# Performance work log

Hardware: AMD Instinct MI355X
Metric: run time of the kernel (lower is better)

Reference implementation:

```python
import jax, jax.numpy as jnp
import numpy as np

N_HEADS = 16
N_EMBD = 1024
HEAD_SIZE = N_EMBD // N_HEADS
B, T = 4, 2048
EPS = 1e-5


def _layernorm(x, g, b):
    mu = jnp.mean(x, axis=-1, keepdims=True)
    var = jnp.mean((x - mu) ** 2, axis=-1, keepdims=True)
    return (x - mu) * jax.lax.rsqrt(var + EPS) * g + b


def setup_inputs() -> dict:
    key = jax.random.key(0)
    ks = jax.random.split(key, 12)
    s_in = 1.0 / np.sqrt(N_EMBD)
    s_ff = 1.0 / np.sqrt(4 * N_EMBD)
    return {
        "x": jax.random.normal(ks[0], (B, T, N_EMBD), jnp.float32),
        "Wq": jax.random.normal(ks[1], (N_HEADS, N_EMBD, HEAD_SIZE), jnp.float32) * s_in,
        "Wk": jax.random.normal(ks[2], (N_HEADS, N_EMBD, HEAD_SIZE), jnp.float32) * s_in,
        "Wv": jax.random.normal(ks[3], (N_HEADS, N_EMBD, HEAD_SIZE), jnp.float32) * s_in,
        "Wproj": jax.random.normal(ks[4], (N_EMBD, N_EMBD), jnp.float32) * s_in,
        "bproj": jnp.zeros((N_EMBD,), jnp.float32),
        "ln1_g": jnp.ones((N_EMBD,), jnp.float32),
        "ln1_b": jnp.zeros((N_EMBD,), jnp.float32),
        "ln2_g": jnp.ones((N_EMBD,), jnp.float32),
        "ln2_b": jnp.zeros((N_EMBD,), jnp.float32),
        "W1": jax.random.normal(ks[5], (N_EMBD, 4 * N_EMBD), jnp.float32) * s_in,
        "b1": jnp.zeros((4 * N_EMBD,), jnp.float32),
        "W2": jax.random.normal(ks[6], (4 * N_EMBD, N_EMBD), jnp.float32) * s_ff,
        "b2": jnp.zeros((N_EMBD,), jnp.float32),
    }


def reference(x, Wq, Wk, Wv, Wproj, bproj, ln1_g, ln1_b, ln2_g, ln2_b, W1, b1, W2, b2):
    Bx, Tx, C = x.shape
    # --- self-attention on ln1(x) ---
    h = _layernorm(x, ln1_g, ln1_b)
    q = jnp.einsum('btc,hcd->bhtd', h, Wq)
    k = jnp.einsum('btc,hcd->bhtd', h, Wk)
    v = jnp.einsum('btc,hcd->bhtd', h, Wv)
    # NOTE: original scales by C**-0.5 where C = n_embd (full dim), not head_size
    scores = jnp.einsum('bhtd,bhsd->bhts', q, k) * (C ** -0.5)
    causal = jnp.tril(jnp.ones((Tx, Tx), dtype=bool))
    scores = jnp.where(causal, scores, -jnp.inf)
    wei = jax.nn.softmax(scores, axis=-1)
    attn = jnp.einsum('bhts,bhsd->bhtd', wei, v)  # [B,H,T,hs]
    attn = attn.transpose(0, 2, 1, 3).reshape(Bx, Tx, -1)  # concat heads -> [B,T,C]
    x = x + attn @ Wproj + bproj
    # --- feed-forward on ln2(x) ---
    h2 = _layernorm(x, ln2_g, ln2_b)
    ff = jax.nn.relu(h2 @ W1 + b1) @ W2 + b2
    return x + ff
```

## Files before the change

kernel.cpp:

```cpp
#include <hip/hip_runtime.h>
#include <math.h>

typedef short bf16x8 __attribute__((ext_vector_type(8)));
typedef float f32x4 __attribute__((ext_vector_type(4)));
typedef unsigned short u16;

__device__ __forceinline__ u16 f2bf(float f) {
    union { float f; unsigned u; } v; v.f = f;
    unsigned r = v.u + 0x7fffu + ((v.u >> 16) & 1u);
    return (u16)(r >> 16);
}

__device__ __forceinline__ void gload_lds16(const void* g, void* l) {
    __builtin_amdgcn_global_load_lds((const __attribute__((address_space(1))) void*)g,
                                     (__attribute__((address_space(3))) void*)l, 16, 0, 0);
}

__global__ __launch_bounds__(256)
void transpose_cvt(const float* __restrict__ in, u16* __restrict__ out, int R, int C)
{
    __shared__ float tile[64][65];
    const size_t slab = (size_t)blockIdx.z * R * C;
    const float* ip = in + slab;
    u16* op = out + slab;
    const int r0 = blockIdx.y * 64, c0 = blockIdx.x * 64;
    const int t = threadIdx.x;
    const int tr = t >> 6, tc = t & 63;
    #pragma unroll
    for (int i = 0; i < 16; ++i)
        tile[tr + i*4][tc] = ip[(size_t)(r0 + tr + i*4)*C + c0 + tc];
    __syncthreads();
    #pragma unroll
    for (int i = 0; i < 16; ++i)
        op[(size_t)(c0 + tr + i*4)*R + r0 + tc] = f2bf(tile[tc][tr + i*4]);
}

__global__ __launch_bounds__(256)
void ln_kernel(const float* __restrict__ x, const float* __restrict__ g,
               const float* __restrict__ b, u16* __restrict__ out)
{
    const int row = blockIdx.x;
    const int t = threadIdx.x;
    const float4 v = ((const float4*)(x + (size_t)row*1024))[t];
    float s = v.x + v.y + v.z + v.w;
    float ss = v.x*v.x + v.y*v.y + v.z*v.z + v.w*v.w;
    #pragma unroll
    for (int m = 1; m < 64; m <<= 1) {
        s  += __shfl_xor(s, m);
        ss += __shfl_xor(ss, m);
    }
    __shared__ float red[8];
    const int wave = t >> 6;
    if ((t & 63) == 0) { red[wave] = s; red[4 + wave] = ss; }
    __syncthreads();
    s  = red[0] + red[1] + red[2] + red[3];
    ss = red[4] + red[5] + red[6] + red[7];
    const float mu = s * (1.f/1024.f);
    const float rs = rsqrtf(ss * (1.f/1024.f) - mu*mu + 1e-5f);
    const float4 gv = ((const float4*)g)[t];
    const float4 bv = ((const float4*)b)[t];
    ushort4 ov;
    ov.x = f2bf((v.x - mu)*rs*gv.x + bv.x);
    ov.y = f2bf((v.y - mu)*rs*gv.y + bv.y);
    ov.z = f2bf((v.z - mu)*rs*gv.z + bv.z);
    ov.w = f2bf((v.w - mu)*rs*gv.w + bv.w);
    ((ushort4*)(out + (size_t)row*1024))[t] = ov;
}

template<int NWG, int N, int K, int EPI>
__global__ __launch_bounds__(256)
void gemm_kernel(const u16* __restrict__ A, const u16* __restrict__ BT,
                 float* __restrict__ out_f32, u16* __restrict__ out_bf16,
                 const float* __restrict__ bias, const float* __restrict__ res,
                 u16* __restrict__ qbuf, u16* __restrict__ kbuf, u16* __restrict__ vt)
{
    __shared__ u16 As[128*32];
    __shared__ u16 Bs[128*32];
    const int bid = blockIdx.x;
    const int tid = ((bid & 7) * (NWG / 8)) + (bid >> 3);
    const int m0 = (tid & 63) * 128;
    const int n0 = (tid >> 6) * 128;
    const int t = threadIdx.x;
    const int wave = t >> 6;
    const int lane = t & 63;
    const int l15 = lane & 15, lg = lane >> 4;
    const int wr = wave >> 1, wc = wave & 1;
    f32x4 acc[4][4] = {};

    const int srow = t >> 2;
    const int sce  = (t & 3) * 8;
    for (int k0 = 0; k0 < K; k0 += 32) {
        #pragma unroll
        for (int i = 0; i < 2; ++i) {
            const u16* ga = A  + (size_t)(m0 + i*64 + srow) * K + k0 + sce;
            const u16* gb = BT + (size_t)(n0 + i*64 + srow) * K + k0 + sce;
            gload_lds16(ga, As + i*2048 + wave*512);
            gload_lds16(gb, Bs + i*2048 + wave*512);
        }
        __syncthreads();
        bf16x8 af[4], bfr[4];
        #pragma unroll
        for (int mi = 0; mi < 4; ++mi)
            af[mi] = *(const bf16x8*)(As + (wr*64 + mi*16 + l15)*32 + lg*8);
        #pragma unroll
        for (int ni = 0; ni < 4; ++ni)
            bfr[ni] = *(const bf16x8*)(Bs + (wc*64 + ni*16 + l15)*32 + lg*8);
        #pragma unroll
        for (int mi = 0; mi < 4; ++mi)
            #pragma unroll
            for (int ni = 0; ni < 4; ++ni)
                acc[mi][ni] = __builtin_amdgcn_mfma_f32_16x16x32_bf16(af[mi], bfr[ni], acc[mi][ni], 0, 0, 0);
        __syncthreads();
    }

    #pragma unroll
    for (int mi = 0; mi < 4; ++mi) {
        #pragma unroll
        for (int ni = 0; ni < 4; ++ni) {
            const int gc = n0 + wc*64 + ni*16 + l15;
            #pragma unroll
            for (int j = 0; j < 4; ++j) {
                const int gr = m0 + wr*64 + mi*16 + lg*4 + j;
                float v = acc[mi][ni][j];
                if constexpr (EPI == 0) {
                    u16 bv = f2bf(v);
                    if (gc < 1024) {
                        qbuf[(size_t)gr*1024 + gc] = bv;
                    } else if (gc < 2048) {
                        kbuf[(size_t)gr*1024 + (gc - 1024)] = bv;
                    } else {
                        const int hd = gc - 2048;
                        const int bb = gr >> 11, tt = gr & 2047;
                        vt[(size_t)((bb*16 + (hd >> 6))*64 + (hd & 63))*2048 + tt] = bv;
                    }
                } else if constexpr (EPI == 1) {
                    out_f32[(size_t)gr*N + gc] = v + bias[gc] + res[(size_t)gr*N + gc];
                } else {
                    out_bf16[(size_t)gr*N + gc] = f2bf(fmaxf(v + bias[gc], 0.f));
                }
            }
        }
    }
}

__device__ __forceinline__ void attn_qtile(
    bf16x8 (&qf)[2][2], f32x4 (&o)[2][4], float (&mprev)[2][4], float (&lsum)[2][4],
    const u16* Ksc, const u16* Vsc, u16* pl,
    int key0, int q0, int l15, int lg, int swzf, int swzp)
{
    #pragma unroll
    for (int mi = 0; mi < 2; ++mi) {
        if (key0 > q0 + mi*16 + 15) continue;
        f32x4 s[4] = {};
        #pragma unroll
        for (int n = 0; n < 4; ++n)
            #pragma unroll
            for (int kk = 0; kk < 2; ++kk) {
                const int row = n*16 + l15;
                bf16x8 kf = *(const bf16x8*)((const char*)Ksc
                                + row*128 + ((kk*64 + lg*16) ^ swzf));
                s[n] = __builtin_amdgcn_mfma_f32_16x16x32_bf16(qf[mi][kk], kf, s[n], 0, 0, 0);
            }
        const bool domask = (key0 + 63) > (q0 + mi*16);
        float tm[4] = {-INFINITY, -INFINITY, -INFINITY, -INFINITY};
        #pragma unroll
        for (int n = 0; n < 4; ++n)
            #pragma unroll
            for (int j = 0; j < 4; ++j) {
                float sv = s[n][j] * 0.03125f;
                if (domask && (key0 + n*16 + l15 > q0 + mi*16 + lg*4 + j)) sv = -INFINITY;
                s[n][j] = sv;
                tm[j] = fmaxf(tm[j], sv);
            }
        #pragma unroll
        for (int m = 1; m < 16; m <<= 1)
            #pragma unroll
            for (int j = 0; j < 4; ++j)
                tm[j] = fmaxf(tm[j], __shfl_xor(tm[j], m, 16));
        float alpha[4], rsum[4];
        #pragma unroll
        for (int j = 0; j < 4; ++j) {
            float mn = fmaxf(mprev[mi][j], tm[j]);
            alpha[j] = __expf(mprev[mi][j] - mn);
            mprev[mi][j] = mn;
            rsum[j] = 0.f;
        }
        #pragma unroll
        for (int n = 0; n < 4; ++n)
            #pragma unroll
            for (int j = 0; j < 4; ++j) {
                float pv = __expf(s[n][j] - mprev[mi][j]);
                rsum[j] += pv;
                const int qq = lg*4 + j;
                pl[qq*64 + ((n*16 + l15) ^ ((qq & 7) * 8))] = f2bf(pv);
            }
        #pragma unroll
        for (int m = 1; m < 16; m <<= 1)
            #pragma unroll
            for (int j = 0; j < 4; ++j)
                rsum[j] += __shfl_xor(rsum[j], m, 16);
        #pragma unroll
        for (int j = 0; j < 4; ++j)
            lsum[mi][j] = lsum[mi][j]*alpha[j] + rsum[j];
        #pragma unroll
        for (int dn = 0; dn < 4; ++dn)
            #pragma unroll
            for (int j = 0; j < 4; ++j)
                o[mi][dn][j] *= alpha[j];
        bf16x8 pf[2];
        #pragma unroll
        for (int kk = 0; kk < 2; ++kk)
            pf[kk] = *(const bf16x8*)(pl + l15*64 + ((kk*32 + lg*8) ^ swzp));
        #pragma unroll
        for (int dn = 0; dn < 4; ++dn)
            #pragma unroll
            for (int kk = 0; kk < 2; ++kk) {
                const int row = dn*16 + l15;
                bf16x8 vf = *(const bf16x8*)((const char*)Vsc
                                + row*128 + ((kk*64 + lg*16) ^ swzf));
                o[mi][dn] = __builtin_amdgcn_mfma_f32_16x16x32_bf16(pf[kk], vf, o[mi][dn], 0, 0, 0);
            }
    }
}

__global__ __launch_bounds__(256, 2)
void attn_kernel(const u16* __restrict__ q, const u16* __restrict__ k,
                 const u16* __restrict__ vt, u16* __restrict__ out)
{
    __shared__ u16 Ks[2][4096];
    __shared__ u16 Vs[2][4096];
    __shared__ u16 Plds[4][1024];

    const int bh = blockIdx.x & 63;
    const int pair = blockIdx.x >> 6;
    const int b = bh >> 4, h = bh & 15;
    const int wave = threadIdx.x >> 6, lane = threadIdx.x & 63;
    const int l15 = lane & 15, lg = lane >> 4;
    const int qA = pair, qB = 15 - pair;
    const int q0A = qA*128 + wave*32;
    const int q0B = qB*128 + wave*32;
    const u16* Qp = q + (size_t)b*2048*1024 + h*64;
    const u16* Kp = k + (size_t)b*2048*1024 + h*64;
    const u16* Vp = vt + (size_t)bh*64*2048;
    u16* pl = Plds[wave];

    bf16x8 qfA[2][2], qfB[2][2];
    #pragma unroll
    for (int mi = 0; mi < 2; ++mi)
        #pragma unroll
        for (int kk = 0; kk < 2; ++kk) {
            qfA[mi][kk] = *(const bf16x8*)(Qp + (size_t)(q0A + mi*16 + l15)*1024 + kk*32 + lg*8);
            qfB[mi][kk] = *(const bf16x8*)(Qp + (size_t)(q0B + mi*16 + l15)*1024 + kk*32 + lg*8);
        }

    const int srow0 = wave*8 + (lane >> 3);
    const int scol  = ((lane & 7) ^ (srow0 & 7)) << 3;
    const int swzf  = (l15 & 7) << 4;
    const int swzp  = (l15 & 7) << 3;

    f32x4 oA[2][4] = {}, oB[2][4] = {};
    float mprevA[2][4], lsumA[2][4], mprevB[2][4], lsumB[2][4];
    #pragma unroll
    for (int mi = 0; mi < 2; ++mi)
        #pragma unroll
        for (int j = 0; j < 4; ++j) {
            mprevA[mi][j] = -INFINITY; lsumA[mi][j] = 0.f;
            mprevB[mi][j] = -INFINITY; lsumB[mi][j] = 0.f;
        }

    const int nkt = 32 - 2*pair;

    #define STAGE(buf, key0_) do { \
        gload_lds16(Kp + (size_t)((key0_) + srow0)*1024 + scol,      &Ks[buf][wave*512]); \
        gload_lds16(Kp + (size_t)((key0_) + srow0 + 32)*1024 + scol, &Ks[buf][(4+wave)*512]); \
        gload_lds16(Vp + (size_t)srow0*2048 + (key0_) + scol,        &Vs[buf][wave*512]); \
        gload_lds16(Vp + (size_t)(srow0+32)*2048 + (key0_) + scol,   &Vs[buf][(4+wave)*512]); \
    } while (0)

    STAGE(0, 0);

    for (int kt = 0; kt < nkt; ++kt) {
        const int cur = kt & 1;
        const int key0 = kt * 64;
        if (kt + 1 < nkt) {
            STAGE(cur ^ 1, key0 + 64);
            asm volatile("s_waitcnt vmcnt(4)" ::: "memory");
        } else {
            asm volatile("s_waitcnt vmcnt(0)" ::: "memory");
        }
        __builtin_amdgcn_s_barrier();
        __builtin_amdgcn_sched_barrier(0);

        if (key0 <= q0A + 31)
            attn_qtile(qfA, oA, mprevA, lsumA, &Ks[cur][0], &Vs[cur][0], pl,
                       key0, q0A, l15, lg, swzf, swzp);
        if (key0 <= q0B + 31)
            attn_qtile(qfB, oB, mprevB, lsumB, &Ks[cur][0], &Vs[cur][0], pl,
                       key0, q0B, l15, lg, swzf, swzp);

        __builtin_amdgcn_sched_barrier(0);
        __builtin_amdgcn_s_barrier();
    }
    #undef STAGE

    #pragma unroll
    for (int mi = 0; mi < 2; ++mi)
        #pragma unroll
        for (int dn = 0; dn < 4; ++dn)
            #pragma unroll
            for (int j = 0; j < 4; ++j) {
                float vA = oA[mi][dn][j] / lsumA[mi][j];
                out[(size_t)(b*2048 + q0A + mi*16 + lg*4 + j)*1024 + h*64 + dn*16 + l15] = f2bf(vA);
                float vB = oB[mi][dn][j] / lsumB[mi][j];
                out[(size_t)(b*2048 + q0B + mi*16 + lg*4 + j)*1024 + h*64 + dn*16 + l15] = f2bf(vB);
            }
}

#define MB(x) ((size_t)(x) << 20)

extern "C" void kernel_launch(void* const* d_in, const int* in_sizes, int n_in,
                              void* d_out, int out_size, void* d_ws, size_t ws_size,
                              hipStream_t stream) {
    const float* x      = (const float*)d_in[0];
    const float* Wq     = (const float*)d_in[1];
    const float* Wk     = (const float*)d_in[2];
    const float* Wv     = (const float*)d_in[3];
    const float* Wproj  = (const float*)d_in[4];
    const float* bproj  = (const float*)d_in[5];
    const float* ln1_g  = (const float*)d_in[6];
    const float* ln1_b  = (const float*)d_in[7];
    const float* ln2_g  = (const float*)d_in[8];
    const float* ln2_b  = (const float*)d_in[9];
    const float* W1     = (const float*)d_in[10];
    const float* b1     = (const float*)d_in[11];
    const float* W2     = (const float*)d_in[12];
    const float* b2     = (const float*)d_in[13];
    float* out = (float*)d_out;

    char* ws = (char*)d_ws;
    u16*  h      = (u16*)(ws + MB(0));
    u16*  qbuf   = (u16*)(ws + MB(16));
    u16*  kbuf   = (u16*)(ws + MB(32));
    u16*  vt     = (u16*)(ws + MB(48));
    u16*  attn   = (u16*)(ws + MB(64));
    float* x2    = (float*)(ws + MB(80));
    u16*  BTqkv  = (u16*)(ws + MB(112));
    u16*  BTproj = (u16*)(ws + MB(118));
    u16*  BT1    = (u16*)(ws + MB(120));
    u16*  BT2    = (u16*)(ws + MB(128));
    u16*  ff     = (u16*)(ws + MB(16));
    u16*  h2     = h;

    transpose_cvt<<<dim3(1,16,16),  256, 0, stream>>>(Wq,    BTqkv,             1024, 64);
    transpose_cvt<<<dim3(1,16,16),  256, 0, stream>>>(Wk,    BTqkv + (1<<20),   1024, 64);
    transpose_cvt<<<dim3(1,16,16),  256, 0, stream>>>(Wv,    BTqkv + (2<<20),   1024, 64);
    transpose_cvt<<<dim3(16,16,1),  256, 0, stream>>>(Wproj, BTproj,            1024, 1024);
    transpose_cvt<<<dim3(64,16,1),  256, 0, stream>>>(W1,    BT1,               1024, 4096);
    transpose_cvt<<<dim3(16,64,1),  256, 0, stream>>>(W2,    BT2,               4096, 1024);

    ln_kernel<<<8192, 256, 0, stream>>>(x, ln1_g, ln1_b, h);
    gemm_kernel<1536,3072,1024,0><<<1536, 256, 0, stream>>>(h, BTqkv, nullptr, nullptr,
        nullptr, nullptr, qbuf, kbuf, vt);
    attn_kernel<<<512, 256, 0, stream>>>(qbuf, kbuf, vt, attn);
    gemm_kernel<512,1024,1024,1><<<512, 256, 0, stream>>>(attn, BTproj, x2, nullptr,
        bproj, x, nullptr, nullptr, nullptr);
    ln_kernel<<<8192, 256, 0, stream>>>(x2, ln2_g, ln2_b, h2);
    gemm_kernel<2048,4096,1024,2><<<2048, 256, 0, stream>>>(h2, BT1, nullptr, ff,
        b1, nullptr, nullptr, nullptr, nullptr);
    gemm_kernel<512,1024,4096,1><<<512, 256, 0, stream>>>(ff, BT2, out, nullptr,
        b2, x2, nullptr, nullptr, nullptr);
}
```

Before: 651.0 us.

## Replace GEMM with 256-row double-buffered, swizzled, ping-pong scheduled kernel

Replaces the 128x128 single-buffered GEMM with a 256xBN tile kernel that uses 512 threads (8 waves), a K-step of 64, double-buffered LDS with XOR-swizzled layout, and a four-phase MFMA schedule using s_setprio and sched barriers. The next K-tile's global-to-LDS load overlaps with compute, and the larger tiles raise data reuse per LDS byte. All four GEMMs switch to it. The cost is higher register and LDS use per block and fewer workgroups (256-512), which may underfill the 256 CUs for the N=1024 GEMMs.

```diff
diff --git a/kernel.cpp b/kernel.cpp
--- a/kernel.cpp
+++ b/kernel.cpp
@@ -67,61 +67,120 @@
     ((ushort4*)(out + (size_t)row*1024))[t] = ov;
 }
 
-template<int NWG, int N, int K, int EPI>
-__global__ __launch_bounds__(256)
-void gemm_kernel(const u16* __restrict__ A, const u16* __restrict__ BT,
-                 float* __restrict__ out_f32, u16* __restrict__ out_bf16,
-                 const float* __restrict__ bias, const float* __restrict__ res,
-                 u16* __restrict__ qbuf, u16* __restrict__ kbuf, u16* __restrict__ vt)
+template<int NWG, int BN, int N, int K, int EPI>
+__global__ __launch_bounds__(512, 2)
+void gemm256_kernel(const u16* __restrict__ A, const u16* __restrict__ BT,
+                    float* __restrict__ out_f32, u16* __restrict__ out_bf16,
+                    const float* __restrict__ bias, const float* __restrict__ res,
+                    u16* __restrict__ qbuf, u16* __restrict__ kbuf, u16* __restrict__ vt)
 {
-    __shared__ u16 As[128*32];
-    __shared__ u16 Bs[128*32];
+    constexpr int NI  = BN / 128;
+    constexpr int WC  = BN / 4;
+    constexpr int SIB = BN / 64;
+    __shared__ u16 As[2][256*64];
+    __shared__ u16 Bs[2][BN*64];
+
     const int bid = blockIdx.x;
     const int tid = ((bid & 7) * (NWG / 8)) + (bid >> 3);
-    const int m0 = (tid & 63) * 128;
-    const int n0 = (tid >> 6) * 128;
+    const int m0 = (tid & 31) * 256;
+    const int n0 = (tid >> 5) * BN;
     const int t = threadIdx.x;
-    const int wave = t >> 6;
     const int lane = t & 63;
     const int l15 = lane & 15, lg = lane >> 4;
-    const int wr = wave >> 1, wc = wave & 1;
-    f32x4 acc[4][4] = {};
-
-    const int srow = t >> 2;
-    const int sce  = (t & 3) * 8;
-    for (int k0 = 0; k0 < K; k0 += 32) {
-        #pragma unroll
-        for (int i = 0; i < 2; ++i) {
-            const u16* ga = A  + (size_t)(m0 + i*64 + srow) * K + k0 + sce;
-            const u16* gb = BT + (size_t)(n0 + i*64 + srow) * K + k0 + sce;
-            gload_lds16(ga, As + i*2048 + wave*512);
-            gload_lds16(gb, Bs + i*2048 + wave*512);
-        }
-        __syncthreads();
-        bf16x8 af[4], bfr[4];
+    const int wid = t >> 6;
+    const int wm = wid >> 2, wn = wid & 3;
+    const int swzf = (l15 & 7) << 4;
+
+    f32x4 acc[2][2][4][NI] = {};
+    bf16x8 af[4][2], b0[NI][2], b1[NI][2];
+
+    const int srow = t >> 3;
+    const int sg8  = ((t & 7) ^ (srow & 7)) * 8;
+
+    #define STAGE_G(BUF, K0) do { \
+        _Pragma("unroll") \
+        for (int i = 0; i < 4; ++i) \
+            gload_lds16(A + (size_t)(m0 + i*64 + srow)*K + (K0) + sg8, &As[BUF][i*4096 + t*8]); \
+        _Pragma("unroll") \
+        for (int i = 0; i < SIB; ++i) \
+            gload_lds16(BT + (size_t)(n0 + i*64 + srow)*K + (K0) + sg8, &Bs[BUF][i*4096 + t*8]); \
+    } while (0)
+
+    #define RD_A(QM) do { \
+        _Pragma("unroll") \
+        for (int mi = 0; mi < 4; ++mi) \
+            _Pragma("unroll") \
+            for (int kk = 0; kk < 2; ++kk) \
+                af[mi][kk] = *(const bf16x8*)((const char*)&As[cur][0] \
+                    + (wm*128 + (QM)*64 + mi*16 + l15)*128 + ((kk*64 + lg*16) ^ swzf)); \
+    } while (0)
+
+    #define RD_B(QN, DST) do { \
+        _Pragma("unroll") \
+        for (int ni = 0; ni < NI; ++ni) \
+            _Pragma("unroll") \
+            for (int kk = 0; kk < 2; ++kk) \
+                DST[ni][kk] = *(const bf16x8*)((const char*)&Bs[cur][0] \
+                    + (wn*WC + (QN)*(WC/2) + ni*16 + l15)*128 + ((kk*64 + lg*16) ^ swzf)); \
+    } while (0)
+
+    #define MFMAQ(QM, QN, BF) do { \
+        _Pragma("unroll") \
+        for (int mi = 0; mi < 4; ++mi) \
+            _Pragma("unroll") \
+            for (int ni = 0; ni < NI; ++ni) \
+                _Pragma("unroll") \
+                for (int kk = 0; kk < 2; ++kk) \
+                    acc[QM][QN][mi][ni] = __builtin_amdgcn_mfma_f32_16x16x32_bf16( \
+                        af[mi][kk], BF[ni][kk], acc[QM][QN][mi][ni], 0, 0, 0); \
+    } while (0)
+
+    #define PHASE_PRE()  do { __builtin_amdgcn_sched_barrier(0); __builtin_amdgcn_s_barrier(); \
+        asm volatile("s_waitcnt lgkmcnt(0)" ::: "memory"); __builtin_amdgcn_sched_barrier(0); \
+        __builtin_amdgcn_s_setprio(1); } while (0)
+    #define PHASE_POST() do { __builtin_amdgcn_s_setprio(0); __builtin_amdgcn_sched_barrier(0); \
+        __builtin_amdgcn_s_barrier(); } while (0)
+
+    STAGE_G(0, 0);
+    asm volatile("s_waitcnt vmcnt(0)" ::: "memory");
+    __builtin_amdgcn_s_barrier();
+
+    const int NKT = K / 64;
+    for (int kt = 0; kt < NKT; ++kt) {
+        const int cur = kt & 1;
+        RD_A(0); RD_B(0, b0);
+        if (kt + 1 < NKT) STAGE_G(cur ^ 1, (kt + 1) * 64);
+        PHASE_PRE();  MFMAQ(0, 0, b0);  PHASE_POST();
+        RD_B(1, b1);
+        PHASE_PRE();  MFMAQ(0, 1, b1);  PHASE_POST();
+        RD_A(1);
+        PHASE_PRE();  MFMAQ(1, 1, b1);  PHASE_POST();
+        asm volatile("s_waitcnt vmcnt(0)" ::: "memory");
+        __builtin_amdgcn_s_barrier();
+        __builtin_amdgcn_s_setprio(1);
+        MFMAQ(1, 0, b0);
+        PHASE_POST();
+    }
+    #undef STAGE_G
+    #undef RD_A
+    #undef RD_B
+    #undef MFMAQ
+    #undef PHASE_PRE
+    #undef PHASE_POST
+
+    #pragma unroll
+    for (int qm = 0; qm < 2; ++qm)
+      #pragma unroll
+      for (int qn = 0; qn < 2; ++qn)
         #pragma unroll
         for (int mi = 0; mi < 4; ++mi)
-            af[mi] = *(const bf16x8*)(As + (wr*64 + mi*16 + l15)*32 + lg*8);
-        #pragma unroll
-        for (int ni = 0; ni < 4; ++ni)
-            bfr[ni] = *(const bf16x8*)(Bs + (wc*64 + ni*16 + l15)*32 + lg*8);
-        #pragma unroll
-        for (int mi = 0; mi < 4; ++mi)
-            #pragma unroll
-            for (int ni = 0; ni < 4; ++ni)
-                acc[mi][ni] = __builtin_amdgcn_mfma_f32_16x16x32_bf16(af[mi], bfr[ni], acc[mi][ni], 0, 0, 0);
-        __syncthreads();
-    }
-
-    #pragma unroll
-    for (int mi = 0; mi < 4; ++mi) {
-        #pragma unroll
-        for (int ni = 0; ni < 4; ++ni) {
-            const int gc = n0 + wc*64 + ni*16 + l15;
+          #pragma unroll
+          for (int ni = 0; ni < NI; ++ni) {
+            const int gc = n0 + wn*WC + qn*(WC/2) + ni*16 + l15;
             #pragma unroll
             for (int j = 0; j < 4; ++j) {
-                const int gr = m0 + wr*64 + mi*16 + lg*4 + j;
-                float v = acc[mi][ni][j];
+                const int gr = m0 + wm*128 + qm*64 + mi*16 + lg*4 + j;
+                float v = acc[qm][qn][mi][ni][j];
                 if constexpr (EPI == 0) {
                     u16 bv = f2bf(v);
                     if (gc < 1024) {
@@ -139,8 +198,7 @@
                     out_bf16[(size_t)gr*N + gc] = f2bf(fmaxf(v + bias[gc], 0.f));
                 }
             }
-        }
-    }
+          }
 }
 
 __device__ __forceinline__ void attn_qtile(
@@ -359,14 +417,14 @@
     transpose_cvt<<<dim3(16,64,1),  256, 0, stream>>>(W2,    BT2,               4096, 1024);
 
     ln_kernel<<<8192, 256, 0, stream>>>(x, ln1_g, ln1_b, h);
-    gemm_kernel<1536,3072,1024,0><<<1536, 256, 0, stream>>>(h, BTqkv, nullptr, nullptr,
+    gemm256_kernel<384,256,3072,1024,0><<<384, 512, 0, stream>>>(h, BTqkv, nullptr, nullptr,
         nullptr, nullptr, qbuf, kbuf, vt);
     attn_kernel<<<512, 256, 0, stream>>>(qbuf, kbuf, vt, attn);
-    gemm_kernel<512,1024,1024,1><<<512, 256, 0, stream>>>(attn, BTproj, x2, nullptr,
+    gemm256_kernel<256,128,1024,1024,1><<<256, 512, 0, stream>>>(attn, BTproj, x2, nullptr,
         bproj, x, nullptr, nullptr, nullptr);
     ln_kernel<<<8192, 256, 0, stream>>>(x2, ln2_g, ln2_b, h2);
-    gemm_kernel<2048,4096,1024,2><<<2048, 256, 0, stream>>>(h2, BT1, nullptr, ff,
+    gemm256_kernel<512,256,4096,1024,2><<<512, 512, 0, stream>>>(h2, BT1, nullptr, ff,
         b1, nullptr, nullptr, nullptr, nullptr);
-    gemm_kernel<512,1024,4096,1><<<512, 256, 0, stream>>>(ff, BT2, out, nullptr,
+    gemm256_kernel<256,128,1024,4096,1><<<256, 512, 0, stream>>>(ff, BT2, out, nullptr,
         b2, x2, nullptr, nullptr, nullptr);
 }
```

New measurement: 655.8 us. Within noise of the previous version (+0.7%).
